# Performance work log

Measured on AMD Instinct MI355X. Metric: run time of the kernel, lower is better.

## Reference

```python
import jax, jax.numpy as jnp
import numpy as np

H, E, L, NH, DH = 1024, 4, 2, 16, 64
B, LP, LS, HF, MAXTOK = 8, 256, 256, 2816, 30
EPS = 1e-5


def setup_inputs() -> dict:
    key = jax.random.key(0)
    ks = jax.random.split(key, 16)
    n = lambda k, sh, s=0.02: jax.random.normal(k, sh, jnp.float32) * s
    return {
        "pose_feat": jax.random.normal(ks[0], (B, LP, H), jnp.float32),
        "scene_feat": jax.random.normal(ks[1], (B, LS, H), jnp.float32),
        # router Mlp: fc1 Linear(H, E), fc2 Linear(E, E) (hidden_features ignored by Mlp)
        "router_fc1_w": n(ks[2], (H, E)), "router_fc1_b": jnp.zeros((E,), jnp.float32),
        "router_fc2_w": n(ks[3], (E, E)), "router_fc2_b": jnp.zeros((E,), jnp.float32),
        # per-expert, per-layer transformer block params, stacked [E, L, ...]
        "attn_norm_w": jnp.ones((E, L, H), jnp.float32),
        "wq_w": n(ks[4], (E, L, H, H)), "wq_b": jnp.zeros((E, L, H), jnp.float32),
        "wk_w": n(ks[5], (E, L, H, H)), "wk_b": jnp.zeros((E, L, H), jnp.float32),
        "wv_w": n(ks[6], (E, L, H, H)), "wv_b": jnp.zeros((E, L, H), jnp.float32),
        "wo_w": n(ks[7], (E, L, H, H)), "wo_b": jnp.zeros((E, L, H), jnp.float32),
        "ffn_norm_w": jnp.ones((E, L, H), jnp.float32),
        "w1_w": n(ks[8], (E, L, H, HF)),
        "w2_w": n(ks[9], (E, L, HF, H)),
        "w3_w": n(ks[10], (E, L, H, HF)),
        # clip_proj2: Linear(H,H) + LayerNorm(H)
        "proj_w": n(ks[11], (H, H)), "proj_b": jnp.zeros((H,), jnp.float32),
        "ln_w": jnp.ones((H,), jnp.float32), "ln_b": jnp.zeros((H,), jnp.float32),
    }


def _rms(x, w):
    # RMSNorm with eps = norm_eps = 1e-5
    return x * jax.lax.rsqrt(jnp.mean(x * x, axis=-1, keepdims=True) + EPS) * w


def _block(x, anw, qw, qb, kw, kb, vw, vb, ow, ob, fnw, w1, w2, w3):
    b, s, _ = x.shape
    xn = _rms(x, anw)
    q = (xn @ qw + qb).reshape(b, s, NH, DH)
    k = (xn @ kw + kb).reshape(b, s, NH, DH)
    v = (xn @ vw + vb).reshape(b, s, NH, DH)
    scores = jnp.einsum("bqhd,bkhd->bhqk", q, k) / (DH ** 0.5)  # non-causal SDPA
    attn = jax.nn.softmax(scores, axis=-1)
    o = jnp.einsum("bhqk,bkhd->bqhd", attn, v).reshape(b, s, NH * DH)
    h = x + o @ ow + ob
    hn = _rms(h, fnw)
    return h + (jax.nn.silu(hn @ w1) * (hn @ w3)) @ w2  # SwiGLU FFN


def _forward(pose_feat, scene_feat, router_fc1_w, router_fc1_b, router_fc2_w, router_fc2_b,
             attn_norm_w, wq_w, wq_b, wk_w, wk_b, wv_w, wv_b, wo_w, wo_b,
             ffn_norm_w, w1_w, w2_w, w3_w, proj_w, proj_b, ln_w, ln_b):
    x = jnp.concatenate((pose_feat, scene_feat), axis=1)  # [B, S, H]
    # router: sigmoid gates normalized to sum to 1 across experts
    r = jax.nn.sigmoid(jax.nn.gelu(x @ router_fc1_w + router_fc1_b, approximate=False) @ router_fc2_w + router_fc2_b)
    r = r / jnp.maximum(jnp.sum(r, axis=-1, keepdims=True), 1e-8)  # [B, S, E]
    keep = min(x.shape[1], MAXTOK)
    combined = jnp.zeros((x.shape[0], keep, H), x.dtype)
    for e in range(E):  # small fixed expert count
        h = x
        for l in range(L):
            h = _block(h, attn_norm_w[e, l], wq_w[e, l], wq_b[e, l], wk_w[e, l], wk_b[e, l],
                       wv_w[e, l], wv_b[e, l], wo_w[e, l], wo_b[e, l],
                       ffn_norm_w[e, l], w1_w[e, l], w2_w[e, l], w3_w[e, l])
        combined = combined + h[:, :keep] * r[:, :keep, e][:, :, None]
    y = combined @ proj_w + proj_b  # clip_proj2 Linear
    mu = jnp.mean(y, axis=-1, keepdims=True)
    var = jnp.var(y, axis=-1, keepdims=True)
    y = (y - mu) * jax.lax.rsqrt(var + EPS) * ln_w + ln_b  # LayerNorm
    return y.reshape(-1, H)


def reference(pose_feat, scene_feat, router_fc1_w, router_fc1_b, router_fc2_w, router_fc2_b,
              attn_norm_w, wq_w, wq_b, wk_w, wk_b, wv_w, wv_b, wo_w, wo_b,
              ffn_norm_w, w1_w, w2_w, w3_w, proj_w, proj_b, ln_w, ln_b):
    return _forward(pose_feat, scene_feat, router_fc1_w, router_fc1_b, router_fc2_w, router_fc2_b,
                    attn_norm_w, wq_w, wq_b, wk_w, wk_b, wv_w, wv_b, wo_w, wo_b,
                    ffn_norm_w, w1_w, w2_w, w3_w, proj_w, proj_b, ln_w, ln_b)
```

## Files before the change

kernel.cpp:

```cpp
#include <hip/hip_runtime.h>
#include <cstdint>
#include <cstddef>

#define HDIM 1024
#define NE 4
#define NL 2
#define NHD 16
#define SEQ 512
#define BATCH 8
#define HFF 2816
#define KEEP 30
#define KEEPT (BATCH*KEEP)
#define TOK (BATCH*SEQ)
#define MKP 256
#define EPSV 1e-5f

typedef __bf16 bf16;
typedef bf16 bf16x8 __attribute__((ext_vector_type(8)));
typedef bf16 bf16x4 __attribute__((ext_vector_type(4)));
typedef float f32x4 __attribute__((ext_vector_type(4)));

__device__ __forceinline__ void gll16(const bf16* g, bf16* l) {
  __builtin_amdgcn_global_load_lds((const __attribute__((address_space(1))) void*)g,
                                   (__attribute__((address_space(3))) void*)l, 16, 0, 0);
}

__global__ __launch_bounds__(256) void k_concat(const float* __restrict__ pose,
                                                const float* __restrict__ scene,
                                                float* __restrict__ x) {
  int idx4 = blockIdx.x * 256 + threadIdx.x;
  int tok = idx4 >> 8;
  int c = (idx4 & 255) << 2;
  int b = tok >> 9, s = tok & 511;
  const float* src = (s < 256) ? (pose + ((size_t)(b*256 + s)*HDIM + c))
                               : (scene + ((size_t)(b*256 + (s-256))*HDIM + c));
  *(f32x4*)(x + (size_t)tok*HDIM + c) = *(const f32x4*)src;
}

__global__ __launch_bounds__(64) void k_router(const float* __restrict__ x,
                                               const float* __restrict__ w1, const float* __restrict__ b1,
                                               const float* __restrict__ w2, const float* __restrict__ b2,
                                               float* __restrict__ r) {
  int row = blockIdx.x;
  int b = row / KEEP, s = row - b*KEEP;
  int lane = threadIdx.x;
  const float* xr = x + (size_t)(b*SEQ + s)*HDIM;
  float p0=0.f, p1=0.f, p2=0.f, p3=0.f;
  for (int k2 = lane; k2 < HDIM; k2 += 64) {
    float xv = xr[k2];
    const float* wr = w1 + k2*4;
    p0 += xv*wr[0]; p1 += xv*wr[1]; p2 += xv*wr[2]; p3 += xv*wr[3];
  }
  #pragma unroll
  for (int off = 32; off; off >>= 1) {
    p0 += __shfl_xor(p0, off); p1 += __shfl_xor(p1, off);
    p2 += __shfl_xor(p2, off); p3 += __shfl_xor(p3, off);
  }
  if (lane == 0) {
    float gg[4] = {p0 + b1[0], p1 + b1[1], p2 + b1[2], p3 + b1[3]};
    #pragma unroll
    for (int i = 0; i < 4; i++) gg[i] = 0.5f*gg[i]*(1.f + erff(gg[i]*0.70710678f));
    float rr[4], sum = 0.f;
    #pragma unroll
    for (int i = 0; i < 4; i++) {
      float a = b2[i];
      #pragma unroll
      for (int j = 0; j < 4; j++) a += gg[j]*w2[j*4 + i];
      rr[i] = 1.f/(1.f + __expf(-a));
      sum += rr[i];
    }
    float inv = 1.f / fmaxf(sum, 1e-8f);
    #pragma unroll
    for (int i = 0; i < 4; i++) r[row*4 + i] = rr[i]*inv;
  }
}

__global__ __launch_bounds__(256) void k_rmsnorm(const float* __restrict__ in,
                                                 const float* __restrict__ w,
                                                 bf16* __restrict__ out) {
  int row = blockIdx.x, tid = threadIdx.x;
  const float* xr = in + (size_t)row*HDIM;
  f32x4 v = *(const f32x4*)(xr + tid*4);
  float ss = v[0]*v[0] + v[1]*v[1] + v[2]*v[2] + v[3]*v[3];
  #pragma unroll
  for (int off = 32; off; off >>= 1) ss += __shfl_xor(ss, off);
  __shared__ float part[4];
  if ((tid & 63) == 0) part[tid >> 6] = ss;
  __syncthreads();
  float scale = rsqrtf((part[0]+part[1]+part[2]+part[3]) * (1.f/HDIM) + EPSV);
  f32x4 wv = *(const f32x4*)(w + tid*4);
  bf16x4 o;
  #pragma unroll
  for (int i = 0; i < 4; i++) o[i] = (bf16)(v[i]*scale*wv[i]);
  *(bf16x4*)(out + (size_t)row*HDIM + tid*4) = o;
}

struct ConvArgs { const float* src[7]; bf16* dst[7]; };
__global__ __launch_bounds__(256) void k_convertT(ConvArgs a) {
  int id = blockIdx.x;
  int t, base;
  if (id < 4096)      { t = id >> 10; base = t << 10; }
  else if (id < 6912) { t = 4; base = 4096; }
  else if (id < 9728) { t = 5; base = 6912; }
  else                { t = 6; base = 9728; }
  int K = (t == 6) ? HFF : HDIM;
  int N = (t == 4 || t == 5) ? HFF : HDIM;
  int tl = id - base;
  int tilesN = N >> 5;
  int tk = tl / tilesN, tn = tl - tk*tilesN;
  __shared__ float tile[32][33];
  int tx = threadIdx.x & 31, ty = threadIdx.x >> 5;
  const float* src = a.src[t];
  bf16* dst = a.dst[t];
  #pragma unroll
  for (int i = 0; i < 4; i++) {
    int rr = ty + i*8;
    tile[rr][tx] = src[(size_t)(tk*32 + rr)*N + tn*32 + tx];
  }
  __syncthreads();
  #pragma unroll
  for (int i = 0; i < 4; i++) {
    int rr = ty + i*8;
    int gr = tn*32 + rr;
    size_t dr;
    if (t == 4)      dr = (size_t)((gr >> 4)*32 + (gr & 15));
    else if (t == 5) dr = (size_t)((gr >> 4)*32 + 16 + (gr & 15));
    else             dr = (size_t)gr;
    dst[dr*K + tk*32 + tx] = (bf16)tile[tx][rr];
  }
}

__global__ __launch_bounds__(256) void k_pack_bias(const float* __restrict__ qb, const float* __restrict__ kb,
                                                   const float* __restrict__ vb, float* __restrict__ dst) {
  int idx = blockIdx.x*256 + threadIdx.x;
  int el = idx / 3072, j = idx - el*3072;
  float v = (j < 1024) ? qb[el*1024 + j]
          : (j < 2048) ? kb[el*1024 + j - 1024]
                       : vb[el*1024 + j - 2048];
  dst[idx] = v;
}


__global__ __launch_bounds__(256) void k_gemm(const bf16* __restrict__ A, const bf16* __restrict__ Bt,
    const float* __restrict__ bias, const float* __restrict__ resid, const bf16* __restrict__ siluSrc,
    float* __restrict__ outF, bf16* __restrict__ outB, int N, int K) {
  __shared__ bf16 As[128*32];
  __shared__ bf16 Bs[128*32];
  int tid = threadIdx.x;
  int wave = tid >> 6, lane = tid & 63;
  int quad = lane >> 4, l16 = lane & 15;
  int wm = (wave >> 1) * 64, wn = (wave & 1) * 64;
  int m0 = blockIdx.y * 128, n0 = blockIdx.x * 128;
  f32x4 zero4 = {0.f, 0.f, 0.f, 0.f};
  f32x4 acc[4][4];
  #pragma unroll
  for (int i = 0; i < 4; i++)
    #pragma unroll
    for (int j = 0; j < 4; j++) acc[i][j] = zero4;
  int srow = wave*32 + (lane >> 2);
  int sg = (lane & 3) ^ ((lane >> 3) & 3);
  int swg = quad ^ ((l16 >> 1) & 3);
  const bf16* Ap = A + (size_t)(m0 + srow)*K + sg*8;
  const bf16* Bp = Bt + (size_t)(n0 + srow)*K + sg*8;
  bf16* AsW = As + wave*1024;
  bf16* BsW = Bs + wave*1024;
  for (int k0 = 0; k0 < K; k0 += 32) {
    __syncthreads();
    gll16(Ap + k0,                AsW);
    gll16(Ap + k0 + (size_t)16*K, AsW + 512);
    gll16(Bp + k0,                BsW);
    gll16(Bp + k0 + (size_t)16*K, BsW + 512);
    __syncthreads();
    bf16x8 af[4], bq[4];
    #pragma unroll
    for (int i = 0; i < 4; i++) af[i] = *(const bf16x8*)&As[(wm + i*16 + l16)*32 + swg*8];
    #pragma unroll
    for (int i = 0; i < 4; i++) bq[i] = *(const bf16x8*)&Bs[(wn + i*16 + l16)*32 + swg*8];
    #pragma unroll
    for (int mi = 0; mi < 4; mi++)
      #pragma unroll
      for (int ni = 0; ni < 4; ni++)
        acc[mi][ni] = __builtin_amdgcn_mfma_f32_16x16x32_bf16(af[mi], bq[ni], acc[mi][ni], 0, 0, 0);
  }
  #pragma unroll
  for (int mi = 0; mi < 4; mi++) {
    #pragma unroll
    for (int ni = 0; ni < 4; ni++) {
      int colg = n0 + wn + ni*16 + l16;
      float bv = bias ? bias[colg] : 0.f;
      #pragma unroll
      for (int rr = 0; rr < 4; rr++) {
        int rowg = m0 + wm + mi*16 + quad*4 + rr;
        size_t off = (size_t)rowg*N + colg;
        float vv = acc[mi][ni][rr] + bv;
        if (resid) vv += resid[off];
        if (siluSrc) { float a = (float)siluSrc[off]; vv *= a / (1.f + __expf(-a)); }
        if (outF) outF[off] = vv;
        else      outB[off] = (bf16)vv;
      }
    }
  }
}

__global__ __launch_bounds__(512, 2) void k_gemm256(const bf16* __restrict__ A, const bf16* __restrict__ Bt,
    const float* __restrict__ bias, bf16* __restrict__ out, int N, int K, int swiglu) {
  __shared__ __align__(16) bf16 As[2][256*32];
  __shared__ __align__(16) bf16 Bs[2][256*32];
  int tid = threadIdx.x;
  int wave = tid >> 6, lane = tid & 63;
  int quad = lane >> 4, l16 = lane & 15;
  int wm128 = (wave >> 2) * 128;
  int wn64  = (wave & 3) * 64;
  int m0 = blockIdx.y * 256, n0 = blockIdx.x * 256;
  int NT = K >> 5;
  f32x4 z = {0.f, 0.f, 0.f, 0.f};
  f32x4 acc[8][4];
  #pragma unroll
  for (int i = 0; i < 8; i++)
    #pragma unroll
    for (int j = 0; j < 4; j++) acc[i][j] = z;
  int sg = (lane & 3) ^ ((lane >> 3) & 3);
  int swg = quad ^ ((l16 >> 1) & 3);
  const bf16* aSrc = A + (size_t)(m0 + wave*16 + (lane>>2))*K + sg*8;
  const bf16* bSrc = Bt + (size_t)(n0 + wave*16 + (lane>>2))*K + sg*8;
  auto stage = [&](int buf, int kt) {
    #pragma unroll
    for (int r = 0; r < 2; r++) {
      gll16(aSrc + (size_t)(r*128)*K + kt*32, &As[buf][(r*128 + wave*16)*32]);
      gll16(bSrc + (size_t)(r*128)*K + kt*32, &Bs[buf][(r*128 + wave*16)*32]);
    }
  };
  stage(0, 0);
  stage(1, 1);
  asm volatile("s_waitcnt vmcnt(4)" ::: "memory");
  asm volatile("s_barrier" ::: "memory");
  for (int kt = 0; kt < NT; ++kt) {
    int cur = kt & 1;
    bf16x8 pb[4];
    {
      bf16x8 pa[4];
      #pragma unroll
      for (int i = 0; i < 4; i++)
        pa[i] = *(const bf16x8*)&As[cur][(wm128 + i*16 + l16)*32 + swg*8];
      #pragma unroll
      for (int i = 0; i < 4; i++)
        pb[i] = *(const bf16x8*)&Bs[cur][(wn64 + i*16 + l16)*32 + swg*8];
      asm volatile("s_barrier" ::: "memory");
      __builtin_amdgcn_s_setprio(1);
      #pragma unroll
      for (int mi = 0; mi < 4; mi++)
        #pragma unroll
        for (int ni = 0; ni < 4; ni++)
          acc[mi][ni] = __builtin_amdgcn_mfma_f32_16x16x32_bf16(pa[mi], pb[ni], acc[mi][ni], 0, 0, 0);
      __builtin_amdgcn_s_setprio(0);
      asm volatile("s_barrier" ::: "memory");
    }
    {
      bf16x8 pa[4];
      #pragma unroll
      for (int i = 0; i < 4; i++)
        pa[i] = *(const bf16x8*)&As[cur][(wm128 + 64 + i*16 + l16)*32 + swg*8];
      asm volatile("s_barrier" ::: "memory");
      __builtin_amdgcn_s_setprio(1);
      #pragma unroll
      for (int mi = 0; mi < 4; mi++)
        #pragma unroll
        for (int ni = 0; ni < 4; ni++)
          acc[4+mi][ni] = __builtin_amdgcn_mfma_f32_16x16x32_bf16(pa[mi], pb[ni], acc[4+mi][ni], 0, 0, 0);
      __builtin_amdgcn_s_setprio(0);
      asm volatile("s_barrier" ::: "memory");
    }
    if (kt + 1 < NT) {
      if (kt + 2 < NT) {
        stage(cur, kt + 2);
        asm volatile("s_waitcnt vmcnt(4)" ::: "memory");
      } else {
        asm volatile("s_waitcnt vmcnt(0)" ::: "memory");
      }
      asm volatile("s_barrier" ::: "memory");
    }
  }
  if (!swiglu) {
    #pragma unroll
    for (int ni = 0; ni < 4; ni++) {
      int colg = n0 + wn64 + ni*16 + l16;
      float bv = bias ? bias[colg] : 0.f;
      #pragma unroll
      for (int mi = 0; mi < 8; mi++)
        #pragma unroll
        for (int rr = 0; rr < 4; rr++) {
          int rowg = m0 + wm128 + mi*16 + quad*4 + rr;
          out[(size_t)rowg*N + colg] = (bf16)(acc[mi][ni][rr] + bv);
        }
    }
  } else {
    int half = N >> 1;
    #pragma unroll
    for (int np = 0; np < 2; np++) {
      int colo = ((n0 + wn64) >> 1) + np*16 + l16;
      #pragma unroll
      for (int mi = 0; mi < 8; mi++)
        #pragma unroll
        for (int rr = 0; rr < 4; rr++) {
          int rowg = m0 + wm128 + mi*16 + quad*4 + rr;
          float xv = acc[mi][np*2][rr];
          float yv = acc[mi][np*2+1][rr];
          out[(size_t)rowg*half + colo] = (bf16)(xv / (1.f + __expf(-xv)) * yv);
        }
    }
  }
}

__global__ __launch_bounds__(256) void k_vtrans(const bf16* __restrict__ v, bf16* __restrict__ vt, int vs) {
  __shared__ bf16 t[64][72];
  int b = blockIdx.z, h = blockIdx.y, s0 = blockIdx.x * 64;
  int r = threadIdx.x >> 2, c0 = (threadIdx.x & 3) * 16;
  const bf16* vp = v + (size_t)(b*SEQ + s0 + r)*vs + h*64 + c0;
  bf16x8 v0 = *(const bf16x8*)vp;
  bf16x8 v1 = *(const bf16x8*)(vp + 8);
  #pragma unroll
  for (int j = 0; j < 8; j++) { t[r][c0+j] = v0[j]; t[r][c0+8+j] = v1[j]; }
  __syncthreads();
  bf16x8 o0, o1;
  #pragma unroll
  for (int j = 0; j < 8; j++) { o0[j] = t[c0+j][r]; o1[j] = t[c0+8+j][r]; }
  bf16* op = vt + ((size_t)(b*NHD + h)*64 + r)*512 + s0 + c0;
  *(bf16x8*)op = o0;
  *(bf16x8*)(op + 8) = o1;
}

__global__ __launch_bounds__(256, 1) void k_attn_mfma(const bf16* __restrict__ q,
    const bf16* __restrict__ k, const bf16* __restrict__ vt,
    bf16* __restrict__ o, int qlen, int orb, int qs) {
  __shared__ bf16 Ps[4][16][520];
  int tid = threadIdx.x;
  int wave = tid >> 6, lane = tid & 63;
  int quad = lane >> 4, l16 = lane & 15;
  int b = blockIdx.z, head = blockIdx.y;
  int q0 = blockIdx.x * 64 + wave * 16;

  const bf16* qp = q + (size_t)(b*SEQ + q0 + l16)*qs + head*64 + quad*8;
  bf16x8 aq0 = *(const bf16x8*)(qp);
  bf16x8 aq1 = *(const bf16x8*)(qp + 32);

  f32x4 z = {0.f, 0.f, 0.f, 0.f};
  f32x4 acc[32];
  #pragma unroll
  for (int ni = 0; ni < 32; ni++) acc[ni] = z;
  const bf16* kb = k + (size_t)(b*SEQ + l16)*qs + head*64 + quad*8;
  #pragma unroll
  for (int ni = 0; ni < 32; ni++) {
    const bf16* kp = kb + (size_t)(ni*16)*qs;
    bf16x8 b0 = *(const bf16x8*)(kp);
    bf16x8 b1 = *(const bf16x8*)(kp + 32);
    acc[ni] = __builtin_amdgcn_mfma_f32_16x16x32_bf16(aq0, b0, acc[ni], 0, 0, 0);
    acc[ni] = __builtin_amdgcn_mfma_f32_16x16x32_bf16(aq1, b1, acc[ni], 0, 0, 0);
  }
  float mx[4] = {-3e30f, -3e30f, -3e30f, -3e30f};
  #pragma unroll
  for (int ni = 0; ni < 32; ni++)
    #pragma unroll
    for (int rr = 0; rr < 4; rr++) {
      float s = acc[ni][rr] * 0.125f;
      acc[ni][rr] = s;
      mx[rr] = fmaxf(mx[rr], s);
    }
  #pragma unroll
  for (int off = 1; off <= 8; off <<= 1)
    #pragma unroll
    for (int rr = 0; rr < 4; rr++)
      mx[rr] = fmaxf(mx[rr], __shfl_xor(mx[rr], off));
  float sm[4] = {0.f, 0.f, 0.f, 0.f};
  #pragma unroll
  for (int ni = 0; ni < 32; ni++)
    #pragma unroll
    for (int rr = 0; rr < 4; rr++) {
      float p = __expf(acc[ni][rr] - mx[rr]);
      acc[ni][rr] = p;
      sm[rr] += p;
    }
  #pragma unroll
  for (int off = 1; off <= 8; off <<= 1)
    #pragma unroll
    for (int rr = 0; rr < 4; rr++)
      sm[rr] += __shfl_xor(sm[rr], off);
  #pragma unroll
  for (int ni = 0; ni < 32; ni++)
    #pragma unroll
    for (int rr = 0; rr < 4; rr++)
      Ps[wave][quad*4 + rr][ni*16 + l16] = (bf16)acc[ni][rr];
  const bf16* vtb = vt + ((size_t)(b*NHD + head)*64 + l16)*512 + quad*8;
  f32x4 accO[4] = {z, z, z, z};
  #pragma unroll 4
  for (int kk = 0; kk < 16; kk++) {
    bf16x8 ap = *(const bf16x8*)&Ps[wave][l16][kk*32 + quad*8];
    #pragma unroll
    for (int ni = 0; ni < 4; ni++) {
      bf16x8 bv = *(const bf16x8*)(vtb + (size_t)(ni*16)*512 + kk*32);
      accO[ni] = __builtin_amdgcn_mfma_f32_16x16x32_bf16(ap, bv, accO[ni], 0, 0, 0);
    }
  }
  float inv[4];
  #pragma unroll
  for (int rr = 0; rr < 4; rr++) inv[rr] = 1.f / sm[rr];
  #pragma unroll
  for (int ni = 0; ni < 4; ni++)
    #pragma unroll
    for (int rr = 0; rr < 4; rr++) {
      int row = q0 + quad*4 + rr;
      if (row < qlen)
        o[(size_t)(b*orb + row)*HDIM + head*64 + ni*16 + l16] = (bf16)(accO[ni][rr] * inv[rr]);
    }
}

__global__ __launch_bounds__(256) void k_gather(const float* __restrict__ h,
                                                float* __restrict__ hk, bf16* __restrict__ ok) {
  int idx = blockIdx.x*256 + threadIdx.x;
  int row = idx >> 10, col = idx & 1023;
  if (row < BATCH*KEEP) {
    int b = row / KEEP, s = row - b*KEEP;
    hk[idx] = h[(size_t)(b*SEQ + s)*HDIM + col];
  } else {
    hk[idx] = 0.f;
    ok[idx] = (bf16)0.f;
  }
}

__global__ __launch_bounds__(256) void k_accum(float* __restrict__ comb, const float* __restrict__ hk,
                                               const float* __restrict__ r, int e, int first) {
  int idx = blockIdx.x*256 + threadIdx.x;
  int row = idx >> 10;
  float vv = hk[idx] * r[row*4 + e];
  comb[idx] = (first ? 0.f : comb[idx]) + vv;
}

__global__ __launch_bounds__(256) void k_proj(const float* __restrict__ comb,
                                              const float* __restrict__ pw,
                                              float* __restrict__ part) {
  int rg = blockIdx.x, ks = blockIdx.y, tid = threadIdx.x;
  __shared__ float xr[8][64];
  for (int i = tid; i < 8*64; i += 256) {
    int r = i >> 6, kk = i & 63;
    xr[r][kk] = comb[(size_t)(rg*8 + r)*HDIM + ks*64 + kk];
  }
  __syncthreads();
  f32x4 acc[8];
  #pragma unroll
  for (int r = 0; r < 8; r++) acc[r] = (f32x4){0.f,0.f,0.f,0.f};
  const float* wp = pw + (size_t)(ks*64)*HDIM + tid*4;
  #pragma unroll 4
  for (int kk = 0; kk < 64; kk++) {
    f32x4 w4 = *(const f32x4*)(wp + (size_t)kk*HDIM);
    #pragma unroll
    for (int r = 0; r < 8; r++) acc[r] += xr[r][kk] * w4;
  }
  #pragma unroll
  for (int r = 0; r < 8; r++)
    *(f32x4*)(part + ((size_t)ks*KEEPT + rg*8 + r)*HDIM + tid*4) = acc[r];
}

__global__ __launch_bounds__(256) void k_ln(const float* __restrict__ part, const float* __restrict__ pb,
    const float* __restrict__ lnw, const float* __restrict__ lnb, float* __restrict__ out) {
  int row = blockIdx.x, tid = threadIdx.x;
  f32x4 acc = *(const f32x4*)(pb + tid*4);
  #pragma unroll
  for (int s = 0; s < 16; s++)
    acc += *(const f32x4*)(part + ((size_t)s*KEEPT + row)*HDIM + tid*4);
  float ps = acc[0]+acc[1]+acc[2]+acc[3];
  #pragma unroll
  for (int off = 32; off; off >>= 1) ps += __shfl_xor(ps, off);
  __shared__ float red1[4], red2[4];
  if ((tid & 63) == 0) red1[tid >> 6] = ps;
  __syncthreads();
  float mu = (red1[0]+red1[1]+red1[2]+red1[3]) * (1.f/HDIM);
  f32x4 d;
  #pragma unroll
  for (int i = 0; i < 4; i++) d[i] = acc[i] - mu;
  float pv = d[0]*d[0]+d[1]*d[1]+d[2]*d[2]+d[3]*d[3];
  #pragma unroll
  for (int off = 32; off; off >>= 1) pv += __shfl_xor(pv, off);
  if ((tid & 63) == 0) red2[tid >> 6] = pv;
  __syncthreads();
  float rs = rsqrtf((red2[0]+red2[1]+red2[2]+red2[3]) * (1.f/HDIM) + EPSV);
  f32x4 lw = *(const f32x4*)(lnw + tid*4);
  f32x4 lb = *(const f32x4*)(lnb + tid*4);
  f32x4 o;
  #pragma unroll
  for (int i = 0; i < 4; i++) o[i] = d[i]*rs*lw[i] + lb[i];
  *(f32x4*)(out + (size_t)row*HDIM + tid*4) = o;
}

extern "C" void kernel_launch(void* const* d_in, const int* in_sizes, int n_in,
                              void* d_out, int out_size, void* d_ws, size_t ws_size,
                              hipStream_t stream) {
  (void)in_sizes; (void)n_in; (void)out_size; (void)ws_size;
  const float* pose = (const float*)d_in[0];
  const float* scene = (const float*)d_in[1];
  const float* rf1w = (const float*)d_in[2];
  const float* rf1b = (const float*)d_in[3];
  const float* rf2w = (const float*)d_in[4];
  const float* rf2b = (const float*)d_in[5];
  const float* anw = (const float*)d_in[6];
  const float* wqw = (const float*)d_in[7];
  const float* wqb = (const float*)d_in[8];
  const float* wkw = (const float*)d_in[9];
  const float* wkb = (const float*)d_in[10];
  const float* wvw = (const float*)d_in[11];
  const float* wvb = (const float*)d_in[12];
  const float* wow = (const float*)d_in[13];
  const float* wob = (const float*)d_in[14];
  const float* fnw = (const float*)d_in[15];
  const float* w1w = (const float*)d_in[16];
  const float* w2w = (const float*)d_in[17];
  const float* w3w = (const float*)d_in[18];
  const float* pw  = (const float*)d_in[19];
  const float* pb  = (const float*)d_in[20];
  const float* lnw = (const float*)d_in[21];
  const float* lnb = (const float*)d_in[22];
  float* out = (float*)d_out;

  char* p = (char*)d_ws;
  auto carve = [&](size_t bytes) { void* r = (void*)p; p += (bytes + 255) & ~(size_t)255; return r; };
  float* x   = (float*)carve((size_t)TOK*HDIM*4);
  float* h   = (float*)carve((size_t)TOK*HDIM*4);
  bf16* xn   = (bf16*)carve((size_t)TOK*HDIM*2);
  bf16* qkv3 = (bf16*)carve((size_t)TOK*3072*2);
  bf16* ob_  = (bf16*)carve((size_t)TOK*HDIM*2);
  bf16* vt   = (bf16*)carve((size_t)TOK*HDIM*2);
  bf16* a1   = (bf16*)carve((size_t)TOK*HFF*2);
  bf16* g    = (bf16*)carve((size_t)TOK*HFF*2);
  bf16* qkvT = (bf16*)carve((size_t)3072*HDIM*2);
  bf16* woT  = (bf16*)carve((size_t)HDIM*HDIM*2);
  bf16* w13T = (bf16*)carve((size_t)2*HDIM*HFF*2);
  bf16* w2T  = (bf16*)carve((size_t)HFF*HDIM*2);
  float* hk  = (float*)carve((size_t)MKP*HDIM*4);
  bf16* hnk  = (bf16*)carve((size_t)MKP*HDIM*2);
  bf16* okb  = (bf16*)carve((size_t)MKP*HDIM*2);
  float* comb = (float*)carve((size_t)KEEPT*HDIM*4);
  float* rbuf = (float*)carve((size_t)KEEPT*4*4);
  float* qkvb = (float*)carve((size_t)8*3072*4);
  float* part = (float*)a1;

  k_concat<<<4096, 256, 0, stream>>>(pose, scene, x);
  k_router<<<KEEPT, 64, 0, stream>>>(x, rf1w, rf1b, rf2w, rf2b, rbuf);
  k_pack_bias<<<96, 256, 0, stream>>>(wqb, wkb, wvb, qkvb);

  for (int e = 0; e < NE; e++) {
    for (int l = 0; l < NL; l++) {
      int el = e*NL + l;
      ConvArgs ca;
      ca.src[0] = wqw + (size_t)el*HDIM*HDIM;
      ca.src[1] = wkw + (size_t)el*HDIM*HDIM;
      ca.src[2] = wvw + (size_t)el*HDIM*HDIM;
      ca.src[3] = wow + (size_t)el*HDIM*HDIM;
      ca.src[4] = w1w + (size_t)el*HDIM*HFF;
      ca.src[5] = w3w + (size_t)el*HDIM*HFF;
      ca.src[6] = w2w + (size_t)el*HFF*HDIM;
      ca.dst[0] = qkvT;
      ca.dst[1] = qkvT + (size_t)1024*HDIM;
      ca.dst[2] = qkvT + (size_t)2048*HDIM;
      ca.dst[3] = woT;
      ca.dst[4] = w13T; ca.dst[5] = w13T; ca.dst[6] = w2T;
      k_convertT<<<12544, 256, 0, stream>>>(ca);

      const float* src_h = (l == 0) ? x : h;
      k_rmsnorm<<<TOK, 256, 0, stream>>>(src_h, anw + (size_t)el*HDIM, xn);
      k_gemm256<<<dim3(12, 16), 512, 0, stream>>>(xn, qkvT, qkvb + (size_t)el*3072, qkv3, 3072, HDIM, 0);
      k_vtrans<<<dim3(8, NHD, BATCH), 256, 0, stream>>>(qkv3 + 2048, vt, 3072);

      if (l == 0) {
        k_attn_mfma<<<dim3(8, NHD, BATCH), 256, 0, stream>>>(qkv3, qkv3 + 1024, vt, ob_, SEQ, SEQ, 3072);
        k_gemm<<<dim3(8, 32), 256, 0, stream>>>(ob_, woT, wob + (size_t)el*HDIM, x, nullptr, h, nullptr, HDIM, HDIM);
        k_rmsnorm<<<TOK, 256, 0, stream>>>(h, fnw + (size_t)el*HDIM, xn);
        k_gemm256<<<dim3(22, 16), 512, 0, stream>>>(xn, w13T, nullptr, g, 2*HFF, HDIM, 1);
        k_gemm<<<dim3(8, 32), 256, 0, stream>>>(g, w2T, nullptr, h, nullptr, h, nullptr, HDIM, HFF);
      } else {
        k_attn_mfma<<<dim3(1, NHD, BATCH), 256, 0, stream>>>(qkv3, qkv3 + 1024, vt, okb, KEEP, KEEP, 3072);
        k_gather<<<1024, 256, 0, stream>>>(h, hk, okb);
        k_gemm<<<dim3(8, 2), 256, 0, stream>>>(okb, woT, wob + (size_t)el*HDIM, hk, nullptr, hk, nullptr, HDIM, HDIM);
        k_rmsnorm<<<MKP, 256, 0, stream>>>(hk, fnw + (size_t)el*HDIM, hnk);
        k_gemm256<<<dim3(22, 1), 512, 0, stream>>>(hnk, w13T, nullptr, g, 2*HFF, HDIM, 1);
        k_gemm<<<dim3(8, 2), 256, 0, stream>>>(g, w2T, nullptr, hk, nullptr, hk, nullptr, HDIM, HFF);
        k_accum<<<960, 256, 0, stream>>>(comb, hk, rbuf, e, (e == 0) ? 1 : 0);
      }
    }
  }
  k_proj<<<dim3(30, 16), 256, 0, stream>>>(comb, pw, part);
  k_ln<<<KEEPT, 256, 0, stream>>>(part, pb, lnw, lnb, out);
}
```

Measured before the change: 2.834 ms.

## Double-buffer k_gemm, add XCD block swizzle, widen weight transpose tiles

k_gemm now double-buffers its LDS tiles and splits each K step into two MFMA halves, with the B and A refills issued after each half so loads overlap compute. k_gemm256 drops the barriers around its LDS fragment reads and splits staging the same way. Both GEMMs remap block IDs with an XCD-aware swizzle so neighbouring tiles land on the same XCD and share L2. The weight convert/transpose kernel moves to 64x64 tiles with vectorized loads and stores, cutting the block count by four. In exchange k_gemm uses twice the LDS, and removing barriers in k_gemm256 depends on the double buffering and wait counts staying correct.

Result: no change. 2.787 ms (-1.7%).

```diff
diff --git a/kernel.cpp b/kernel.cpp
--- a/kernel.cpp
+++ b/kernel.cpp
@@ -23,6 +23,12 @@
 __device__ __forceinline__ void gll16(const bf16* g, bf16* l) {
   __builtin_amdgcn_global_load_lds((const __attribute__((address_space(1))) void*)g,
                                    (__attribute__((address_space(3))) void*)l, 16, 0, 0);
+}
+
+__device__ __forceinline__ int xcd_swz(int orig, int nwg) {
+  int q = nwg >> 3, r = nwg & 7;
+  int xcd = orig & 7, loc = orig >> 3;
+  return (xcd < r ? xcd*(q+1) : r*(q+1) + (xcd-r)*q) + loc;
 }
 
 __global__ __launch_bounds__(256) void k_concat(const float* __restrict__ pose,
@@ -99,35 +105,39 @@
 __global__ __launch_bounds__(256) void k_convertT(ConvArgs a) {
   int id = blockIdx.x;
   int t, base;
-  if (id < 4096)      { t = id >> 10; base = t << 10; }
-  else if (id < 6912) { t = 4; base = 4096; }
-  else if (id < 9728) { t = 5; base = 6912; }
-  else                { t = 6; base = 9728; }
+  if (id < 1024)      { t = id >> 8; base = t << 8; }
+  else if (id < 1728) { t = 4; base = 1024; }
+  else if (id < 2432) { t = 5; base = 1728; }
+  else                { t = 6; base = 2432; }
   int K = (t == 6) ? HFF : HDIM;
   int N = (t == 4 || t == 5) ? HFF : HDIM;
   int tl = id - base;
-  int tilesN = N >> 5;
+  int tilesN = N >> 6;
   int tk = tl / tilesN, tn = tl - tk*tilesN;
-  __shared__ float tile[32][33];
-  int tx = threadIdx.x & 31, ty = threadIdx.x >> 5;
+  __shared__ float tile[64][68];
   const float* src = a.src[t];
   bf16* dst = a.dst[t];
+  int c4 = (threadIdx.x & 15) * 4;
+  int r0 = threadIdx.x >> 4;
   #pragma unroll
   for (int i = 0; i < 4; i++) {
-    int rr = ty + i*8;
-    tile[rr][tx] = src[(size_t)(tk*32 + rr)*N + tn*32 + tx];
+    int rr = r0 + i*16;
+    *(f32x4*)&tile[rr][c4] = *(const f32x4*)&src[(size_t)(tk*64 + rr)*N + tn*64 + c4];
   }
   __syncthreads();
-  #pragma unroll
-  for (int i = 0; i < 4; i++) {
-    int rr = ty + i*8;
-    int gr = tn*32 + rr;
-    size_t dr;
-    if (t == 4)      dr = (size_t)((gr >> 4)*32 + (gr & 15));
-    else if (t == 5) dr = (size_t)((gr >> 4)*32 + 16 + (gr & 15));
-    else             dr = (size_t)gr;
-    dst[dr*K + tk*32 + tx] = (bf16)tile[tx][rr];
-  }
+  int n = threadIdx.x >> 2;
+  int kb = (threadIdx.x & 3) * 16;
+  int gr = tn*64 + n;
+  size_t dr;
+  if (t == 4)      dr = (size_t)((gr >> 4)*32 + (gr & 15));
+  else if (t == 5) dr = (size_t)((gr >> 4)*32 + 16 + (gr & 15));
+  else             dr = (size_t)gr;
+  bf16* dp = dst + dr*K + tk*64 + kb;
+  bf16x8 o0, o1;
+  #pragma unroll
+  for (int j = 0; j < 8; j++) { o0[j] = (bf16)tile[kb+j][n]; o1[j] = (bf16)tile[kb+8+j][n]; }
+  *(bf16x8*)dp = o0;
+  *(bf16x8*)(dp+8) = o1;
 }
 
 __global__ __launch_bounds__(256) void k_pack_bias(const float* __restrict__ qb, const float* __restrict__ kb,
@@ -144,13 +154,16 @@
 __global__ __launch_bounds__(256) void k_gemm(const bf16* __restrict__ A, const bf16* __restrict__ Bt,
     const float* __restrict__ bias, const float* __restrict__ resid, const bf16* __restrict__ siluSrc,
     float* __restrict__ outF, bf16* __restrict__ outB, int N, int K) {
-  __shared__ bf16 As[128*32];
-  __shared__ bf16 Bs[128*32];
+  __shared__ __align__(16) bf16 As[2][128*32];
+  __shared__ __align__(16) bf16 Bs[2][128*32];
   int tid = threadIdx.x;
   int wave = tid >> 6, lane = tid & 63;
   int quad = lane >> 4, l16 = lane & 15;
   int wm = (wave >> 1) * 64, wn = (wave & 1) * 64;
-  int m0 = blockIdx.y * 128, n0 = blockIdx.x * 128;
+  int nwg = gridDim.x * gridDim.y;
+  int wg = xcd_swz(blockIdx.y * gridDim.x + blockIdx.x, nwg);
+  int bx = wg % gridDim.x, by = wg / gridDim.x;
+  int m0 = by * 128, n0 = bx * 128;
   f32x4 zero4 = {0.f, 0.f, 0.f, 0.f};
   f32x4 acc[4][4];
   #pragma unroll
@@ -162,25 +175,52 @@
   int swg = quad ^ ((l16 >> 1) & 3);
   const bf16* Ap = A + (size_t)(m0 + srow)*K + sg*8;
   const bf16* Bp = Bt + (size_t)(n0 + srow)*K + sg*8;
-  bf16* AsW = As + wave*1024;
-  bf16* BsW = Bs + wave*1024;
-  for (int k0 = 0; k0 < K; k0 += 32) {
-    __syncthreads();
-    gll16(Ap + k0,                AsW);
-    gll16(Ap + k0 + (size_t)16*K, AsW + 512);
-    gll16(Bp + k0,                BsW);
-    gll16(Bp + k0 + (size_t)16*K, BsW + 512);
-    __syncthreads();
-    bf16x8 af[4], bq[4];
-    #pragma unroll
-    for (int i = 0; i < 4; i++) af[i] = *(const bf16x8*)&As[(wm + i*16 + l16)*32 + swg*8];
-    #pragma unroll
-    for (int i = 0; i < 4; i++) bq[i] = *(const bf16x8*)&Bs[(wn + i*16 + l16)*32 + swg*8];
-    #pragma unroll
-    for (int mi = 0; mi < 4; mi++)
+  auto stageA = [&](int buf, int kt) {
+    gll16(Ap + (size_t)kt*32,                &As[buf][wave*1024]);
+    gll16(Ap + (size_t)kt*32 + (size_t)16*K, &As[buf][wave*1024 + 512]);
+  };
+  auto stageB = [&](int buf, int kt) {
+    gll16(Bp + (size_t)kt*32,                &Bs[buf][wave*1024]);
+    gll16(Bp + (size_t)kt*32 + (size_t)16*K, &Bs[buf][wave*1024 + 512]);
+  };
+  int NT = K >> 5;
+  stageA(0, 0); stageB(0, 0);
+  stageA(1, 1); stageB(1, 1);
+  asm volatile("s_waitcnt vmcnt(4)" ::: "memory");
+  asm volatile("s_barrier" ::: "memory");
+  for (int kt = 0; kt < NT; ++kt) {
+    int cur = kt & 1;
+    bf16x8 pb[4], pa[2];
+    #pragma unroll
+    for (int i = 0; i < 4; i++) pb[i] = *(const bf16x8*)&Bs[cur][(wn + i*16 + l16)*32 + swg*8];
+    #pragma unroll
+    for (int i = 0; i < 2; i++) pa[i] = *(const bf16x8*)&As[cur][(wm + i*16 + l16)*32 + swg*8];
+    __builtin_amdgcn_s_setprio(1);
+    #pragma unroll
+    for (int mi = 0; mi < 2; mi++)
       #pragma unroll
       for (int ni = 0; ni < 4; ni++)
-        acc[mi][ni] = __builtin_amdgcn_mfma_f32_16x16x32_bf16(af[mi], bq[ni], acc[mi][ni], 0, 0, 0);
+        acc[mi][ni] = __builtin_amdgcn_mfma_f32_16x16x32_bf16(pa[mi], pb[ni], acc[mi][ni], 0, 0, 0);
+    __builtin_amdgcn_s_setprio(0);
+    asm volatile("s_barrier" ::: "memory");
+    if (kt + 2 < NT) stageB(cur, kt + 2);
+    bf16x8 pa2[2];
+    #pragma unroll
+    for (int i = 0; i < 2; i++) pa2[i] = *(const bf16x8*)&As[cur][(wm + 32 + i*16 + l16)*32 + swg*8];
+    __builtin_amdgcn_s_setprio(1);
+    #pragma unroll
+    for (int mi = 0; mi < 2; mi++)
+      #pragma unroll
+      for (int ni = 0; ni < 4; ni++)
+        acc[2+mi][ni] = __builtin_amdgcn_mfma_f32_16x16x32_bf16(pa2[mi], pb[ni], acc[2+mi][ni], 0, 0, 0);
+    __builtin_amdgcn_s_setprio(0);
+    asm volatile("s_barrier" ::: "memory");
+    if (kt + 2 < NT) stageA(cur, kt + 2);
+    if (kt + 1 < NT) {
+      if (kt + 2 < NT) asm volatile("s_waitcnt vmcnt(4)" ::: "memory");
+      else             asm volatile("s_waitcnt vmcnt(0)" ::: "memory");
+      asm volatile("s_barrier" ::: "memory");
+    }
   }
   #pragma unroll
   for (int mi = 0; mi < 4; mi++) {
@@ -211,7 +251,10 @@
   int quad = lane >> 4, l16 = lane & 15;
   int wm128 = (wave >> 2) * 128;
   int wn64  = (wave & 3) * 64;
-  int m0 = blockIdx.y * 256, n0 = blockIdx.x * 256;
+  int nwg = gridDim.x * gridDim.y;
+  int wg = xcd_swz(blockIdx.y * gridDim.x + blockIdx.x, nwg);
+  int bx = wg % gridDim.x, by = wg / gridDim.x;
+  int m0 = by * 256, n0 = bx * 256;
   int NT = K >> 5;
   f32x4 z = {0.f, 0.f, 0.f, 0.f};
   f32x4 acc[8][4];
@@ -223,60 +266,54 @@
   int swg = quad ^ ((l16 >> 1) & 3);
   const bf16* aSrc = A + (size_t)(m0 + wave*16 + (lane>>2))*K + sg*8;
   const bf16* bSrc = Bt + (size_t)(n0 + wave*16 + (lane>>2))*K + sg*8;
-  auto stage = [&](int buf, int kt) {
-    #pragma unroll
-    for (int r = 0; r < 2; r++) {
-      gll16(aSrc + (size_t)(r*128)*K + kt*32, &As[buf][(r*128 + wave*16)*32]);
-      gll16(bSrc + (size_t)(r*128)*K + kt*32, &Bs[buf][(r*128 + wave*16)*32]);
-    }
+  auto stageA = [&](int buf, int kt) {
+    #pragma unroll
+    for (int r = 0; r < 2; r++)
+      gll16(aSrc + (size_t)(r*128)*K + (size_t)kt*32, &As[buf][(r*128 + wave*16)*32]);
   };
-  stage(0, 0);
-  stage(1, 1);
+  auto stageB = [&](int buf, int kt) {
+    #pragma unroll
+    for (int r = 0; r < 2; r++)
+      gll16(bSrc + (size_t)(r*128)*K + (size_t)kt*32, &Bs[buf][(r*128 + wave*16)*32]);
+  };
+  stageA(0, 0); stageB(0, 0);
+  stageA(1, 1); stageB(1, 1);
   asm volatile("s_waitcnt vmcnt(4)" ::: "memory");
   asm volatile("s_barrier" ::: "memory");
   for (int kt = 0; kt < NT; ++kt) {
     int cur = kt & 1;
-    bf16x8 pb[4];
-    {
-      bf16x8 pa[4];
-      #pragma unroll
-      for (int i = 0; i < 4; i++)
-        pa[i] = *(const bf16x8*)&As[cur][(wm128 + i*16 + l16)*32 + swg*8];
-      #pragma unroll
-      for (int i = 0; i < 4; i++)
-        pb[i] = *(const bf16x8*)&Bs[cur][(wn64 + i*16 + l16)*32 + swg*8];
-      asm volatile("s_barrier" ::: "memory");
-      __builtin_amdgcn_s_setprio(1);
-      #pragma unroll
-      for (int mi = 0; mi < 4; mi++)
-        #pragma unroll
-        for (int ni = 0; ni < 4; ni++)
-          acc[mi][ni] = __builtin_amdgcn_mfma_f32_16x16x32_bf16(pa[mi], pb[ni], acc[mi][ni], 0, 0, 0);
-      __builtin_amdgcn_s_setprio(0);
-      asm volatile("s_barrier" ::: "memory");
-    }
-    {
-      bf16x8 pa[4];
-      #pragma unroll
-      for (int i = 0; i < 4; i++)
-        pa[i] = *(const bf16x8*)&As[cur][(wm128 + 64 + i*16 + l16)*32 + swg*8];
-      asm volatile("s_barrier" ::: "memory");
-      __builtin_amdgcn_s_setprio(1);
-      #pragma unroll
-      for (int mi = 0; mi < 4; mi++)
-        #pragma unroll
-        for (int ni = 0; ni < 4; ni++)
-          acc[4+mi][ni] = __builtin_amdgcn_mfma_f32_16x16x32_bf16(pa[mi], pb[ni], acc[4+mi][ni], 0, 0, 0);
-      __builtin_amdgcn_s_setprio(0);
-      asm volatile("s_barrier" ::: "memory");
-    }
+    bf16x8 pb[4], pa[4];
+    #pragma unroll
+    for (int i = 0; i < 4; i++)
+      pa[i] = *(const bf16x8*)&As[cur][(wm128 + i*16 + l16)*32 + swg*8];
+    #pragma unroll
+    for (int i = 0; i < 4; i++)
+      pb[i] = *(const bf16x8*)&Bs[cur][(wn64 + i*16 + l16)*32 + swg*8];
+    __builtin_amdgcn_s_setprio(1);
+    #pragma unroll
+    for (int mi = 0; mi < 4; mi++)
+      #pragma unroll
+      for (int ni = 0; ni < 4; ni++)
+        acc[mi][ni] = __builtin_amdgcn_mfma_f32_16x16x32_bf16(pa[mi], pb[ni], acc[mi][ni], 0, 0, 0);
+    __builtin_amdgcn_s_setprio(0);
+    asm volatile("s_barrier" ::: "memory");
+    if (kt + 2 < NT) stageB(cur, kt + 2);
+    bf16x8 pa2[4];
+    #pragma unroll
+    for (int i = 0; i < 4; i++)
+      pa2[i] = *(const bf16x8*)&As[cur][(wm128 + 64 + i*16 + l16)*32 + swg*8];
+    __builtin_amdgcn_s_setprio(1);
+    #pragma unroll
+    for (int mi = 0; mi < 4; mi++)
+      #pragma unroll
+      for (int ni = 0; ni < 4; ni++)
+        acc[4+mi][ni] = __builtin_amdgcn_mfma_f32_16x16x32_bf16(pa2[mi], pb[ni], acc[4+mi][ni], 0, 0, 0);
+    __builtin_amdgcn_s_setprio(0);
+    asm volatile("s_barrier" ::: "memory");
+    if (kt + 2 < NT) stageA(cur, kt + 2);
     if (kt + 1 < NT) {
-      if (kt + 2 < NT) {
-        stage(cur, kt + 2);
-        asm volatile("s_waitcnt vmcnt(4)" ::: "memory");
-      } else {
-        asm volatile("s_waitcnt vmcnt(0)" ::: "memory");
-      }
+      if (kt + 2 < NT) asm volatile("s_waitcnt vmcnt(4)" ::: "memory");
+      else             asm volatile("s_waitcnt vmcnt(0)" ::: "memory");
       asm volatile("s_barrier" ::: "memory");
     }
   }
@@ -561,7 +598,7 @@
       ca.dst[2] = qkvT + (size_t)2048*HDIM;
       ca.dst[3] = woT;
       ca.dst[4] = w13T; ca.dst[5] = w13T; ca.dst[6] = w2T;
-      k_convertT<<<12544, 256, 0, stream>>>(ca);
+      k_convertT<<<3136, 256, 0, stream>>>(ca);
 
       const float* src_h = (l == 0) ? x : h;
       k_rmsnorm<<<TOK, 256, 0, stream>>>(src_h, anw + (size_t)el*HDIM, xn);
```
